# Optimization experiments

Measured on AMD Instinct MI355X. Metric: run time of the kernel, lower is better.

## Reference

```python
import jax, jax.numpy as jnp
import numpy as np
import math

TOKEN_DIM = 1024
NUM_HEADS = 16
HEAD_DIM = TOKEN_DIM // NUM_HEADS
T, B, N = 32, 32, 64


def setup_inputs() -> dict:
    key = jax.random.key(0)
    ks = jax.random.split(key, 9)
    query_vec = jax.random.normal(ks[0], (T, B, TOKEN_DIM), dtype=jnp.float32)
    tokens = jax.random.normal(ks[1], (T, B, N, TOKEN_DIM), dtype=jnp.float32)
    gate_logits = jax.random.normal(ks[2], (T, B, N), dtype=jnp.float32)
    scale = 1.0 / math.sqrt(TOKEN_DIM)
    Wq = jax.random.normal(ks[3], (TOKEN_DIM, TOKEN_DIM), dtype=jnp.float32) * scale
    Wk = jax.random.normal(ks[4], (TOKEN_DIM, TOKEN_DIM), dtype=jnp.float32) * scale
    Wv = jax.random.normal(ks[5], (TOKEN_DIM, TOKEN_DIM), dtype=jnp.float32) * scale
    bq = jnp.zeros((TOKEN_DIM,), dtype=jnp.float32)
    bk = jnp.zeros((TOKEN_DIM,), dtype=jnp.float32)
    bv = jnp.zeros((TOKEN_DIM,), dtype=jnp.float32)
    return {"query_vec": query_vec, "tokens": tokens, "gate_logits": gate_logits,
            "Wq": Wq, "bq": bq, "Wk": Wk, "bk": bk, "Wv": Wv, "bv": bv}


def reference(query_vec, tokens, gate_logits, Wq, bq, Wk, bk, Wv, bv):
    # QKV projections
    q = query_vec @ Wq + bq                      # [T,B,D]
    k = tokens @ Wk + bk                         # [T,B,N,D]
    v = tokens @ Wv + bv                         # [T,B,N,D]
    q = q.reshape(T, B, NUM_HEADS, HEAD_DIM)
    k = k.reshape(T, B, N, NUM_HEADS, HEAD_DIM)
    v = v.reshape(T, B, N, NUM_HEADS, HEAD_DIM)
    logits = jnp.einsum('tbhd,tbnhd->tbhn', q, k) / math.sqrt(HEAD_DIM)
    logits = logits + gate_logits[:, :, None, :]
    attn = jax.nn.softmax(logits, axis=-1)       # [T,B,H,N]
    attended = jnp.einsum('tbhn,tbnhd->tbhd', attn, v)
    attended = attended.reshape(T, B, TOKEN_DIM)
    mean_attn = attn.mean(axis=2)                # [T,B,N]
    return (attended, mean_attn, logits)
```

## Files before the change

### kernel.cpp

```cpp
#include <hip/hip_runtime.h>
#include <hip/hip_bf16.h>
#include <hip/hip_cooperative_groups.h>

namespace cg = cooperative_groups;

typedef __attribute__((ext_vector_type(4))) float f32x4;
typedef __attribute__((ext_vector_type(8))) short bf16x8;
typedef unsigned int u32;
typedef unsigned short u16;

#define DEV static __device__ __forceinline__


DEV u16 f2bf(float x){
  union { float f; u32 u; } v; v.f = x;
  u32 r = v.u + 0x7FFFu + ((v.u >> 16) & 1u);
  return (u16)(r >> 16);
}
DEV float bf2f(u16 s){
  union { u32 u; float f; } v; v.u = ((u32)s) << 16;
  return v.f;
}

#define MFMA16(a,b,c) __builtin_amdgcn_mfma_f32_16x16x32_bf16((a),(b),(c),0,0,0)

DEV int tok_off(int n, int dbyte){ return n*2048 + (dbyte ^ ((n & 7) << 4)); }

#define SWZ(n) ((((n)&3)<<5) | ((((n)>>2)&1)<<4))

DEV void bar_lgkm(){
  __builtin_amdgcn_sched_barrier(0);
  asm volatile("s_waitcnt lgkmcnt(0)" ::: "memory");
  __builtin_amdgcn_s_barrier();
  __builtin_amdgcn_sched_barrier(0);
}

DEV bf16x8 cvt8(f32x4 lo, f32x4 hi){
  union { u32 u[4]; bf16x8 v; } r;
  asm("v_cvt_pk_bf16_f32 %0, %1, %2" : "=v"(r.u[0]) : "v"(lo.x), "v"(lo.y));
  asm("v_cvt_pk_bf16_f32 %0, %1, %2" : "=v"(r.u[1]) : "v"(lo.z), "v"(lo.w));
  asm("v_cvt_pk_bf16_f32 %0, %1, %2" : "=v"(r.u[2]) : "v"(hi.x), "v"(hi.y));
  asm("v_cvt_pk_bf16_f32 %0, %1, %2" : "=v"(r.u[3]) : "v"(hi.z), "v"(hi.w));
  return r.v;
}

DEV void stage8(const float* __restrict__ tokens, int tbn, int tk0,
                char* smem, int bb, int w, int l){
  char* ldsb = smem + (size_t)bb*32768 + (size_t)w*8192;
  const char* gb = (const char*)tokens + (size_t)tbn*262144 + (size_t)tk0*4096;
  #pragma unroll
  for (int j = 0; j < 8; ++j){
    const int nloc  = w*2 + (j >> 2);
    const int inner = (((j & 3)*1024) + l*16) ^ SWZ(nloc);
    __builtin_amdgcn_global_load_lds(
        (const __attribute__((address_space(1))) u32*)(gb + (size_t)nloc*4096 + inner),
        (__attribute__((address_space(3))) u32*)(ldsb + j*1024),
        16, 0, 0);
  }
}

#define MEGA_DYN_LDS 65536

__global__ __launch_bounds__(256, 2) void k_mega(
    const float* __restrict__ qv, const float* __restrict__ tokens,
    const float* __restrict__ gate,
    const float* __restrict__ Wq, const float* __restrict__ bq,
    const float* __restrict__ Wk, const float* __restrict__ bk,
    const float* __restrict__ Wv, const float* __restrict__ bv,
    u16* __restrict__ qvB, u16* __restrict__ WqT, u16* __restrict__ WkB,
    u16* __restrict__ WvT, float* __restrict__ qf, u16* __restrict__ qb,
    u16* __restrict__ U, u16* __restrict__ ctxb,
    float* __restrict__ out_att, float* __restrict__ out_mean,
    float* __restrict__ out_logits){
  extern __shared__ __align__(16) char smem[];
  __shared__ __align__(16) char sstat[10496];
  cg::grid_group grid = cg::this_grid();
  const int tid = threadIdx.x;
  const int bx  = blockIdx.x;
  const int l = tid & 63, w = tid >> 6, g = l >> 4, li = l & 15;

  {
    const f32x4* s4 = (const f32x4*)qv;
    uint2* d2 = (uint2*)qvB;
    int g0 = bx*256 + tid;
    #pragma unroll
    for (int i = 0; i < 2; ++i){
      int idx = g0 + i*131072;
      f32x4 v = s4[idx];
      uint2 pk;
      pk.x = (u32)f2bf(v.x) | ((u32)f2bf(v.y) << 16);
      pk.y = (u32)f2bf(v.z) | ((u32)f2bf(v.w) << 16);
      d2[idx] = pk;
    }
  }
  {
    u16 (*tile)[65] = (u16 (*)[65])sstat;
    for (int tl = bx; tl < 768; tl += 512){
      __syncthreads();
      const int which = tl >> 8, t8 = tl & 255;
      const float* src = which==0 ? Wq : (which==1 ? Wk : Wv);
      const int bi = (t8 >> 4) << 6, bj = (t8 & 15) << 6;
      #pragma unroll
      for (int k2 = 0; k2 < 16; ++k2){
        int e = tid + (k2 << 8); int r = e >> 6, c = e & 63;
        tile[r][c] = f2bf(src[(size_t)(bi + r)*1024 + bj + c]);
      }
      __syncthreads();
      if (which == 1){
        #pragma unroll
        for (int k2 = 0; k2 < 16; ++k2){
          int e = tid + (k2 << 8); int r = e >> 6, c = e & 63;
          WkB[(size_t)(bi + r)*1024 + bj + c] = tile[r][c];
        }
      } else {
        u16* dst = which==0 ? WqT : WvT;
        #pragma unroll
        for (int k2 = 0; k2 < 16; ++k2){
          int e = tid + (k2 << 8); int r = e >> 6, c = e & 63;
          dst[(size_t)(bj + r)*1024 + bi + c] = tile[c][r];
        }
      }
    }
  }
  __threadfence(); grid.sync(); __threadfence();

  {
    const int wm = w & 1, wn = w >> 1;
    const int m_base = (bx >> 5)*64 + wm*32;
    const int n_base = (bx & 31)*32 + wn*16;
    f32x4 acc[2]; acc[0] = (f32x4)0.0f; acc[1] = (f32x4)0.0f;
    #pragma unroll 4
    for (int kb = 0; kb < 32; ++kb){
      const int k0 = kb*32 + g*8;
      bf16x8 b = *(const bf16x8*)(WqT + (size_t)(n_base + li)*1024 + k0);
      #pragma unroll
      for (int rt = 0; rt < 2; ++rt){
        bf16x8 a = *(const bf16x8*)(qvB + (size_t)(m_base + rt*16 + li)*1024 + k0);
        acc[rt] = MFMA16(a, b, acc[rt]);
      }
    }
    #pragma unroll
    for (int rt = 0; rt < 2; ++rt)
      #pragma unroll
      for (int r = 0; r < 4; ++r){
        int m = m_base + rt*16 + g*4 + r;
        int n = n_base + li;
        float val = acc[rt][r] + bq[n];
        qf[(size_t)m*1024 + n] = val;
        qb[(size_t)m*1024 + n] = f2bf(val);
      }
  }
  __threadfence(); grid.sync(); __threadfence();

  {
    u16 (*stile)[64] = (u16 (*)[64])sstat;
    const int wm = w & 1, wn = w >> 1;
    for (int i = 0; i < 8; ++i){
      const int tl = bx*8 + i;
      const int tb0 = (tl >> 8)*64, d0 = ((tl >> 4) & 15)*64, h = tl & 15;
      f32x4 acc[2][2];
      #pragma unroll
      for (int a0=0;a0<2;++a0)
        #pragma unroll
        for (int b0=0;b0<2;++b0) acc[a0][b0] = (f32x4)0.0f;
      #pragma unroll
      for (int kb = 0; kb < 2; ++kb){
        const int k0 = h*64 + kb*32 + g*8;
        bf16x8 a[2], b[2];
        #pragma unroll
        for (int rt=0;rt<2;++rt)
          a[rt] = *(const bf16x8*)(qb + (size_t)(tb0 + wm*32 + rt*16 + li)*1024 + k0);
        #pragma unroll
        for (int ct=0;ct<2;++ct)
          b[ct] = *(const bf16x8*)(WkB + (size_t)(d0 + wn*32 + ct*16 + li)*1024 + k0);
        #pragma unroll
        for (int rt=0;rt<2;++rt)
          #pragma unroll
          for (int ct=0;ct<2;++ct)
            acc[rt][ct] = MFMA16(a[rt], b[ct], acc[rt][ct]);
      }
      __syncthreads();
      #pragma unroll
      for (int rt=0;rt<2;++rt)
        #pragma unroll
        for (int ct=0;ct<2;++ct)
          #pragma unroll
          for (int r=0;r<4;++r)
            stile[wm*32 + rt*16 + g*4 + r][wn*32 + ct*16 + li] = f2bf(acc[rt][ct][r]);
      __syncthreads();
      const int rr = tid >> 2, cg4 = tid & 3;
      f32x4* dst = (f32x4*)(U + ((size_t)(tb0 + rr)*16 + h)*1024 + d0 + cg4*16);
      const f32x4* s4 = (const f32x4*)(&stile[rr][cg4*16]);
      dst[0] = s4[0]; dst[1] = s4[1];
    }
  }
  __threadfence(); grid.sync(); __threadfence();

  {
    float* part_s   = (float*)(sstat);
    float* logits_s = (float*)(sstat + 4096);
    float* p_s      = (float*)(sstat + 8192);
    float* csum     = (float*)(sstat + 10240);
    float* r_s      = (float*)(sstat + 10304);
    float* mzs      = (float*)(sstat + 10368);
    const int sh = tid >> 4, sj = tid & 15;

    __syncthreads();
    stage8(tokens, bx, 0, smem, 0, w, l);

    float m_run = -1e30f, z_run = 0.0f;
    f32x4 cacc[4][4];
    bf16x8 a[8];

    for (int r = 0; r < 16; ++r){
      const int c = r & 7, n0 = c*8;
      const int tb = bx + (r >> 3)*512;
      char* bufc = smem + (size_t)(r & 1)*32768;

      __syncthreads();
      if (r + 1 < 16)
        stage8(tokens, bx + ((r+1) >> 3)*512, ((r+1) & 7)*8, smem, (r+1) & 1, w, l);

      if (c == 0){
        m_run = -1e30f; z_run = 0.0f;
        #pragma unroll
        for (int i=0;i<4;++i)
          #pragma unroll
          for (int j=0;j<4;++j) cacc[i][j] = (f32x4)0.0f;
        const bf16x8* Ub = (const bf16x8*)(U + (size_t)tb*16384);
        #pragma unroll
        for (int i = 0; i < 8; ++i)
          a[i] = Ub[li*128 + (w*8 + i)*4 + g];
        const float* qp = qf + (size_t)tb*1024 + sh*64 + sj*4;
        const float* bp = bk + sh*64 + sj*4;
        float part = qp[0]*bp[0] + qp[1]*bp[1] + qp[2]*bp[2] + qp[3]*bp[3];
        part += __shfl_xor(part, 1); part += __shfl_xor(part, 2);
        part += __shfl_xor(part, 4); part += __shfl_xor(part, 8);
        if (sj == 0) csum[sh] = part;
      }

      {
        const int row = li & 7;
        const int sw  = SWZ(row);
        f32x4 acc = (f32x4)0.0f;
        #pragma unroll
        for (int i = 0; i < 8; ++i){
          const int p0b = (w*8 + i)*128 + g*32;
          f32x4 lo = *(const f32x4*)(bufc + row*4096 + ((p0b     ) ^ sw));
          f32x4 hi = *(const f32x4*)(bufc + row*4096 + ((p0b + 16) ^ sw));
          acc = MFMA16(a[i], cvt8(lo, hi), acc);
        }
        *(f32x4*)(part_s + (size_t)(w*64 + l)*4) = acc;
      }
      bar_lgkm();

      if (sj < 8){
        const int idx = ((sh >> 2)*16 + sj)*4 + (sh & 3);
        float lv = part_s[idx] + part_s[256 + idx] + part_s[512 + idx] + part_s[768 + idx];
        lv = (lv + csum[sh])*0.125f + gate[(size_t)tb*64 + n0 + sj];
        logits_s[sh*64 + n0 + sj] = lv;
        out_logits[(size_t)tb*1024 + sh*64 + n0 + sj] = lv;
        float cm = lv;
        cm = fmaxf(cm, __shfl_xor(cm, 1));
        cm = fmaxf(cm, __shfl_xor(cm, 2));
        cm = fmaxf(cm, __shfl_xor(cm, 4));
        float m_new = fmaxf(m_run, cm);
        float rsc = __expf(m_run - m_new);
        float p0 = __expf(lv - m_new);
        float zs = p0;
        zs += __shfl_xor(zs, 1); zs += __shfl_xor(zs, 2); zs += __shfl_xor(zs, 4);
        z_run = z_run * rsc + zs;
        m_run = m_new;
        p_s[sj*16 + sh] = p0;
        if (sj == 0){
          r_s[sh] = rsc;
          if (c == 7){ mzs[sh*2] = m_new; mzs[sh*2 + 1] = 1.0f / z_run; }
        }
      }
      bar_lgkm();

      {
        float rr4[4];
        #pragma unroll
        for (int hh = 0; hh < 4; ++hh) rr4[hh] = r_s[w*4 + hh];
        #pragma unroll
        for (int dq = 0; dq < 4; ++dq)
          #pragma unroll
          for (int hh = 0; hh < 4; ++hh) cacc[dq][hh] *= rr4[hh];
        #pragma unroll
        for (int nl = 0; nl < 8; ++nl){
          const f32x4 p = *(const f32x4*)(p_s + nl*16 + w*4);
          const int swn = SWZ(nl);
          #pragma unroll
          for (int dq = 0; dq < 4; ++dq){
            const f32x4 t = *(const f32x4*)(bufc + (size_t)nl*4096 + ((dq*1024 + l*16) ^ swn));
            #pragma unroll
            for (int hh = 0; hh < 4; ++hh)
              cacc[dq][hh] += t * p[hh];
          }
        }
      }

      if (c == 7){
        if (tid < 64){
          float s = 0.0f;
          #pragma unroll
          for (int h = 0; h < 16; ++h)
            s += __expf(logits_s[h*64 + tid] - mzs[h*2]) * mzs[h*2 + 1];
          out_mean[(size_t)tb*64 + tid] = s * 0.0625f;
        }
        #pragma unroll
        for (int hh = 0; hh < 4; ++hh){
          const int h = w*4 + hh;
          const float zinv = mzs[h*2 + 1];
          #pragma unroll
          for (int dq = 0; dq < 4; ++dq){
            f32x4 v = cacc[dq][hh];
            uint2 pk;
            pk.x = (u32)f2bf(v.x * zinv) | ((u32)f2bf(v.y * zinv) << 16);
            pk.y = (u32)f2bf(v.z * zinv) | ((u32)f2bf(v.w * zinv) << 16);
            *(uint2*)(ctxb + ((size_t)tb*16 + h)*1024 + dq*256 + l*4) = pk;
          }
        }
      }
    }
  }
  __threadfence(); grid.sync(); __threadfence();

  {
    const int wm = w & 1, wn = w >> 1;
    const int m_base = (bx >> 4)*32, h = bx & 15;
    f32x4 acc[2]; acc[0] = (f32x4)0.0f; acc[1] = (f32x4)0.0f;
    #pragma unroll 4
    for (int kb = 0; kb < 32; ++kb){
      const int k0 = kb*32 + g*8;
      bf16x8 a = *(const bf16x8*)(ctxb + ((size_t)(m_base + wm*16 + li)*16 + h)*1024 + k0);
      #pragma unroll
      for (int ct = 0; ct < 2; ++ct){
        bf16x8 b = *(const bf16x8*)(WvT + (size_t)(h*64 + wn*32 + ct*16 + li)*1024 + k0);
        acc[ct] = MFMA16(a, b, acc[ct]);
      }
    }
    #pragma unroll
    for (int ct = 0; ct < 2; ++ct)
      #pragma unroll
      for (int r = 0; r < 4; ++r){
        int m = m_base + wm*16 + g*4 + r;
        int dout = h*64 + wn*32 + ct*16 + li;
        out_att[(size_t)m*1024 + dout] = acc[ct][r] + bv[dout];
      }
  }
}

__global__ __launch_bounds__(256) void k_convert(
    const float* __restrict__ Wq, const float* __restrict__ Wk, const float* __restrict__ Wv,
    u16* __restrict__ WqT, u16* __restrict__ WkB, u16* __restrict__ WvT){
  __shared__ u16 tile[64][65];
  const int which = blockIdx.y;
  const float* src = which==0 ? Wq : (which==1 ? Wk : Wv);
  const int bi = (blockIdx.x >> 4) << 6;
  const int bj = (blockIdx.x & 15) << 6;
  const int t  = threadIdx.x;
  #pragma unroll
  for (int k2 = 0; k2 < 16; ++k2){
    int e = t + (k2 << 8);
    int r = e >> 6, c = e & 63;
    tile[r][c] = f2bf(src[(size_t)(bi + r)*1024 + bj + c]);
  }
  __syncthreads();
  if (which == 1){
    #pragma unroll
    for (int k2 = 0; k2 < 16; ++k2){
      int e = t + (k2 << 8); int r = e >> 6, c = e & 63;
      WkB[(size_t)(bi + r)*1024 + bj + c] = tile[r][c];
    }
  } else {
    u16* dst = which==0 ? WqT : WvT;
    #pragma unroll
    for (int k2 = 0; k2 < 16; ++k2){
      int e = t + (k2 << 8); int r = e >> 6, c = e & 63;
      dst[(size_t)(bj + r)*1024 + bi + c] = tile[c][r];
    }
  }
}

__global__ __launch_bounds__(256) void k_qproj(
    const float* __restrict__ qv, const u16* __restrict__ WqT, const float* __restrict__ bq,
    float* __restrict__ qf, u16* __restrict__ qb){
  const int l = threadIdx.x & 63, w = threadIdx.x >> 6;
  const int wm = w & 1, wn = w >> 1;
  const int g = l >> 4, li = l & 15;
  const int m_base = blockIdx.x*64 + wm*32;
  const int n_base = blockIdx.y*64 + wn*32;
  f32x4 acc[2][2];
  #pragma unroll
  for (int i=0;i<2;++i)
    #pragma unroll
    for (int j=0;j<2;++j) acc[i][j] = (f32x4)0.0f;

  #pragma unroll 4
  for (int kb = 0; kb < 32; ++kb){
    const int k0 = kb*32 + g*8;
    bf16x8 a[2], b[2];
    #pragma unroll
    for (int rt = 0; rt < 2; ++rt){
      const float* p = qv + (size_t)(m_base + rt*16 + li)*1024 + k0;
      f32x4 lo = *(const f32x4*)p;
      f32x4 hi = *(const f32x4*)(p+4);
      union { u16 s[8]; bf16x8 v; } u;
      u.s[0]=f2bf(lo.x); u.s[1]=f2bf(lo.y); u.s[2]=f2bf(lo.z); u.s[3]=f2bf(lo.w);
      u.s[4]=f2bf(hi.x); u.s[5]=f2bf(hi.y); u.s[6]=f2bf(hi.z); u.s[7]=f2bf(hi.w);
      a[rt] = u.v;
    }
    #pragma unroll
    for (int ct = 0; ct < 2; ++ct)
      b[ct] = *(const bf16x8*)(WqT + (size_t)(n_base + ct*16 + li)*1024 + k0);
    #pragma unroll
    for (int rt = 0; rt < 2; ++rt)
      #pragma unroll
      for (int ct = 0; ct < 2; ++ct)
        acc[rt][ct] = MFMA16(a[rt], b[ct], acc[rt][ct]);
  }
  #pragma unroll
  for (int rt=0;rt<2;++rt)
    #pragma unroll
    for (int ct=0;ct<2;++ct)
      #pragma unroll
      for (int r=0;r<4;++r){
        int m = m_base + rt*16 + g*4 + r;
        int n = n_base + ct*16 + li;
        float val = acc[rt][ct][r] + bq[n];
        qf[(size_t)m*1024 + n] = val;
        qb[(size_t)m*1024 + n] = f2bf(val);
      }
}

__global__ __launch_bounds__(256) void k_umat(
    const u16* __restrict__ qb, const u16* __restrict__ WkB, u16* __restrict__ U){
  __shared__ __align__(16) u16 stile[64][64];
  const int l = threadIdx.x & 63, w = threadIdx.x >> 6;
  const int wm = w & 1, wn = w >> 1, g = l >> 4, li = l & 15;
  const int tb0 = blockIdx.x*64, d0 = blockIdx.y*64, h = blockIdx.z;
  f32x4 acc[2][2];
  #pragma unroll
  for (int i=0;i<2;++i)
    #pragma unroll
    for (int j=0;j<2;++j) acc[i][j] = (f32x4)0.0f;

  #pragma unroll
  for (int kb = 0; kb < 2; ++kb){
    const int k0 = h*64 + kb*32 + g*8;
    bf16x8 a[2], b[2];
    #pragma unroll
    for (int rt=0;rt<2;++rt)
      a[rt] = *(const bf16x8*)(qb + (size_t)(tb0 + wm*32 + rt*16 + li)*1024 + k0);
    #pragma unroll
    for (int ct=0;ct<2;++ct)
      b[ct] = *(const bf16x8*)(WkB + (size_t)(d0 + wn*32 + ct*16 + li)*1024 + k0);
    #pragma unroll
    for (int rt=0;rt<2;++rt)
      #pragma unroll
      for (int ct=0;ct<2;++ct)
        acc[rt][ct] = MFMA16(a[rt], b[ct], acc[rt][ct]);
  }
  #pragma unroll
  for (int rt=0;rt<2;++rt)
    #pragma unroll
    for (int ct=0;ct<2;++ct)
      #pragma unroll
      for (int r=0;r<4;++r)
        stile[wm*32 + rt*16 + g*4 + r][wn*32 + ct*16 + li] = f2bf(acc[rt][ct][r]);
  __syncthreads();
  const int r = threadIdx.x >> 2, cg4 = threadIdx.x & 3;
  f32x4* dst = (f32x4*)(U + ((size_t)(tb0 + r)*16 + h)*1024 + d0 + cg4*16);
  const f32x4* s4 = (const f32x4*)(&stile[r][cg4*16]);
  dst[0] = s4[0]; dst[1] = s4[1];
}

#define K3_LDS 76032
__global__ __launch_bounds__(256, 2) void k_attn(
    const float* __restrict__ tokens, const float* __restrict__ gate,
    const u16* __restrict__ U, const float* __restrict__ qf, const float* __restrict__ bk,
    float* __restrict__ out_logits, float* __restrict__ out_mean, u16* __restrict__ ctx){
  extern __shared__ __align__(16) char smem[];
  float* part_s   = (float*)(smem + 65536);
  float* logits_s = (float*)(smem + 69632);
  float* p_s      = (float*)(smem + 73728);
  float* csum     = (float*)(smem + 75776);
  float* r_s      = (float*)(smem + 75840);
  float* mzs      = (float*)(smem + 75904);
  const int tb = blockIdx.x;
  const int tid = threadIdx.x;
  const int l = tid & 63, w = tid >> 6, g = l >> 4, li = l & 15;
  const int nt = w & 1, kh = w >> 1;
  const int sh = tid >> 4, sj = tid & 15;

  bf16x8 a[16];
  const bf16x8* Ub = (const bf16x8*)(U + (size_t)tb*16384);
  #pragma unroll
  for (int i = 0; i < 16; ++i)
    a[i] = Ub[li*128 + (kh*16 + i)*4 + g];

  {
    const float* qp = qf + (size_t)tb*1024 + sh*64 + sj*4;
    const float* bp = bk + sh*64 + sj*4;
    float part = qp[0]*bp[0] + qp[1]*bp[1] + qp[2]*bp[2] + qp[3]*bp[3];
    part += __shfl_xor(part, 1); part += __shfl_xor(part, 2);
    part += __shfl_xor(part, 4); part += __shfl_xor(part, 8);
    if (sj == 0) csum[sh] = part;
  }

  float m_run = -1e30f, z_run = 0.0f;
  f32x4 cacc[4][4];
  #pragma unroll
  for (int i=0;i<4;++i)
    #pragma unroll
    for (int j=0;j<4;++j) cacc[i][j] = (f32x4)0.0f;

  const f32x4* src4 = (const f32x4*)(tokens + (size_t)tb*65536);

  for (int c = 0; c < 2; ++c){
    const int n0 = c*32;
    __syncthreads();
    #pragma unroll 8
    for (int it = 0; it < 32; ++it){
      f32x4 v = src4[(size_t)(n0 + it)*256 + tid];
      uint2 pk;
      pk.x = (u32)f2bf(v.x) | ((u32)f2bf(v.y) << 16);
      pk.y = (u32)f2bf(v.z) | ((u32)f2bf(v.w) << 16);
      *(uint2*)(smem + tok_off(it, tid*8)) = pk;
    }
    __syncthreads();
    {
      f32x4 acc = (f32x4)0.0f;
      #pragma unroll
      for (int i = 0; i < 16; ++i){
        int kb = kh*16 + i;
        bf16x8 b = *(const bf16x8*)(smem + tok_off(nt*16 + li, (kb*32 + g*8)*2));
        acc = MFMA16(a[i], b, acc);
      }
      *(f32x4*)(part_s + (size_t)(w*64 + l)*4) = acc;
      __syncthreads();
      if (kh == 0){
        acc += *(const f32x4*)(part_s + (size_t)((w+2)*64 + l)*4);
        float gv = gate[(size_t)tb*64 + n0 + nt*16 + li];
        #pragma unroll
        for (int r = 0; r < 4; ++r){
          int h = g*4 + r;
          logits_s[h*64 + n0 + nt*16 + li] = (acc[r] + csum[h])*0.125f + gv;
        }
      }
      __syncthreads();
    }
    {
      float lv0 = logits_s[sh*64 + n0 + sj];
      float lv1 = logits_s[sh*64 + n0 + 16 + sj];
      out_logits[(size_t)tb*1024 + sh*64 + n0 + sj]      = lv0;
      out_logits[(size_t)tb*1024 + sh*64 + n0 + 16 + sj] = lv1;
      float cm = fmaxf(lv0, lv1);
      cm = fmaxf(cm, __shfl_xor(cm, 1)); cm = fmaxf(cm, __shfl_xor(cm, 2));
      cm = fmaxf(cm, __shfl_xor(cm, 4)); cm = fmaxf(cm, __shfl_xor(cm, 8));
      float m_new = fmaxf(m_run, cm);
      float rsc = __expf(m_run - m_new);
      float p0 = __expf(lv0 - m_new), p1 = __expf(lv1 - m_new);
      float zs = p0 + p1;
      zs += __shfl_xor(zs, 1); zs += __shfl_xor(zs, 2);
      zs += __shfl_xor(zs, 4); zs += __shfl_xor(zs, 8);
      z_run = z_run * rsc + zs;
      m_run = m_new;
      p_s[sj*16 + sh]        = p0;
      p_s[(sj + 16)*16 + sh] = p1;
      if (sj == 0){
        r_s[sh] = rsc;
        if (c == 1){ mzs[sh*2] = m_new; mzs[sh*2 + 1] = 1.0f / z_run; }
      }
    }
    __syncthreads();
    {
      float rr[4];
      #pragma unroll
      for (int hh = 0; hh < 4; ++hh) rr[hh] = r_s[w*4 + hh];
      #pragma unroll
      for (int dq = 0; dq < 4; ++dq)
        #pragma unroll
        for (int hh = 0; hh < 4; ++hh) cacc[dq][hh] *= rr[hh];
      for (int nl = 0; nl < 32; ++nl){
        f32x4 p = *(const f32x4*)(p_s + nl*16 + w*4);
        #pragma unroll
        for (int dq = 0; dq < 4; ++dq){
          uint2 t2 = *(const uint2*)(smem + tok_off(nl, (dq*256 + l*4)*2));
          float f0 = bf2f((u16)(t2.x & 0xFFFFu));
          float f1 = bf2f((u16)(t2.x >> 16));
          float f2 = bf2f((u16)(t2.y & 0xFFFFu));
          float f3 = bf2f((u16)(t2.y >> 16));
          #pragma unroll
          for (int hh = 0; hh < 4; ++hh){
            float av = p[hh];
            cacc[dq][hh].x += av*f0; cacc[dq][hh].y += av*f1;
            cacc[dq][hh].z += av*f2; cacc[dq][hh].w += av*f3;
          }
        }
      }
    }
  }

  if (tid < 64){
    float s = 0.0f;
    #pragma unroll
    for (int h = 0; h < 16; ++h)
      s += __expf(logits_s[h*64 + tid] - mzs[h*2]) * mzs[h*2 + 1];
    out_mean[(size_t)tb*64 + tid] = s * 0.0625f;
  }

  #pragma unroll
  for (int hh = 0; hh < 4; ++hh){
    const int h = w*4 + hh;
    const float zinv = mzs[h*2 + 1];
    #pragma unroll
    for (int dq = 0; dq < 4; ++dq){
      f32x4 v = cacc[dq][hh];
      uint2 pk;
      pk.x = (u32)f2bf(v.x * zinv) | ((u32)f2bf(v.y * zinv) << 16);
      pk.y = (u32)f2bf(v.z * zinv) | ((u32)f2bf(v.w * zinv) << 16);
      *(uint2*)(ctx + ((size_t)tb*16 + h)*1024 + dq*256 + l*4) = pk;
    }
  }
}

__global__ __launch_bounds__(256) void k_attended(
    const u16* __restrict__ ctx, const u16* __restrict__ WvT, const float* __restrict__ bv,
    float* __restrict__ out_att){
  const int l = threadIdx.x & 63, w = threadIdx.x >> 6;
  const int wm = w & 1, wn = w >> 1, g = l >> 4, li = l & 15;
  const int tb0 = blockIdx.x*64, h = blockIdx.y;
  f32x4 acc[2][2];
  #pragma unroll
  for (int i=0;i<2;++i)
    #pragma unroll
    for (int j=0;j<2;++j) acc[i][j] = (f32x4)0.0f;

  #pragma unroll 4
  for (int kb = 0; kb < 32; ++kb){
    const int k0 = kb*32 + g*8;
    bf16x8 a[2], b[2];
    #pragma unroll
    for (int rt=0;rt<2;++rt)
      a[rt] = *(const bf16x8*)(ctx + ((size_t)(tb0 + wm*32 + rt*16 + li)*16 + h)*1024 + k0);
    #pragma unroll
    for (int ct=0;ct<2;++ct)
      b[ct] = *(const bf16x8*)(WvT + (size_t)(h*64 + wn*32 + ct*16 + li)*1024 + k0);
    #pragma unroll
    for (int rt=0;rt<2;++rt)
      #pragma unroll
      for (int ct=0;ct<2;++ct)
        acc[rt][ct] = MFMA16(a[rt], b[ct], acc[rt][ct]);
  }
  #pragma unroll
  for (int rt=0;rt<2;++rt)
    #pragma unroll
    for (int ct=0;ct<2;++ct)
      #pragma unroll
      for (int r=0;r<4;++r){
        int m = tb0 + wm*32 + rt*16 + g*4 + r;
        int dout = h*64 + wn*32 + ct*16 + li;
        out_att[(size_t)m*1024 + dout] = acc[rt][ct][r] + bv[dout];
      }
}

extern "C" void kernel_launch(void* const* d_in, const int* in_sizes, int n_in,
                              void* d_out, int out_size, void* d_ws, size_t ws_size,
                              hipStream_t stream){
  const float* qv     = (const float*)d_in[0];
  const float* tokens = (const float*)d_in[1];
  const float* gate   = (const float*)d_in[2];
  const float* Wq     = (const float*)d_in[3];
  const float* bq     = (const float*)d_in[4];
  const float* Wk     = (const float*)d_in[5];
  const float* bk     = (const float*)d_in[6];
  const float* Wv     = (const float*)d_in[7];
  const float* bv     = (const float*)d_in[8];

  char* ws = (char*)d_ws;
  u16*   qvB = (u16*)(ws);
  u16*   WqT = (u16*)(ws + (2u<<20));
  u16*   WkB = (u16*)(ws + (4u<<20));
  u16*   WvT = (u16*)(ws + (6u<<20));
  float* qf  = (float*)(ws + (8u<<20));
  u16*   qb  = (u16*)(ws + (12u<<20));
  u16*   U   = (u16*)(ws + (14u<<20));
  u16*   ctxb= (u16*)(ws + (46u<<20));

  float* out_att    = (float*)d_out;
  float* out_mean   = out_att + 1048576;
  float* out_logits = out_att + 1114112;

  int dev = 0; (void)hipGetDevice(&dev);
  int coop = 0; (void)hipDeviceGetAttribute(&coop, hipDeviceAttributeCooperativeLaunch, dev);
  int ncu = 0;  (void)hipDeviceGetAttribute(&ncu, hipDeviceAttributeMultiprocessorCount, dev);
  int perCU = 0;
  hipError_t oe = hipOccupancyMaxActiveBlocksPerMultiprocessor(
                      &perCU, (const void*)k_mega, 256, (size_t)MEGA_DYN_LDS);
  bool use_coop = (coop != 0) && (oe == hipSuccess) && ((long)perCU * (long)ncu >= 512);

  if (use_coop){
    void* args[] = { (void*)&qv, (void*)&tokens, (void*)&gate,
                     (void*)&Wq, (void*)&bq, (void*)&Wk, (void*)&bk,
                     (void*)&Wv, (void*)&bv,
                     (void*)&qvB, (void*)&WqT, (void*)&WkB, (void*)&WvT,
                     (void*)&qf, (void*)&qb, (void*)&U, (void*)&ctxb,
                     (void*)&out_att, (void*)&out_mean, (void*)&out_logits };
    hipError_t le = hipLaunchCooperativeKernel((const void*)k_mega, dim3(512), dim3(256),
                                               args, MEGA_DYN_LDS, stream);
    if (le == hipSuccess) return;
    use_coop = false;
  }

  (void)hipFuncSetAttribute((const void*)k_attn,
                            hipFuncAttributeMaxDynamicSharedMemorySize, K3_LDS);
  k_convert <<<dim3(256, 3),    256, 0,      stream>>>(Wq, Wk, Wv, WqT, WkB, WvT);
  k_qproj   <<<dim3(16, 16),    256, 0,      stream>>>(qv, WqT, bq, qf, qb);
  k_umat    <<<dim3(16, 16, 16),256, 0,      stream>>>(qb, WkB, U);
  k_attn    <<<dim3(1024),      256, K3_LDS, stream>>>(tokens, gate, U, qf, bk,
                                                       out_logits, out_mean, ctxb);
  k_attended<<<dim3(16, 16),    256, 0,      stream>>>(ctxb, WvT, bv, out_att);
}
```

Baseline: 177.3 us.

## Replace cooperative megakernel with multi-kernel path using async fp32 token staging

Removes the cooperative-launch megakernel and its grid-wide syncs, so the separate kernel sequence (convert, qproj, umat, attn, attended) always runs. The k_attn kernel now streams fp32 tokens into a double-buffered LDS with direct global-to-LDS loads in 8-token chunks and converts to bf16 inside the MFMA path, instead of converting synchronously in 32-token chunks. Each block now handles one tb rather than two in a persistent loop, with more blocks in flight. The trade-off is extra kernel launch boundaries in place of grid syncs.

```diff
diff --git a/kernel.cpp b/kernel.cpp
--- a/kernel.cpp
+++ b/kernel.cpp
@@ -1,8 +1,5 @@
 #include <hip/hip_runtime.h>
 #include <hip/hip_bf16.h>
-#include <hip/hip_cooperative_groups.h>
-
-namespace cg = cooperative_groups;
 
 typedef __attribute__((ext_vector_type(4))) float f32x4;
 typedef __attribute__((ext_vector_type(8))) short bf16x8;
@@ -24,13 +21,17 @@
 
 #define MFMA16(a,b,c) __builtin_amdgcn_mfma_f32_16x16x32_bf16((a),(b),(c),0,0,0)
 
-DEV int tok_off(int n, int dbyte){ return n*2048 + (dbyte ^ ((n & 7) << 4)); }
-
 #define SWZ(n) ((((n)&3)<<5) | ((((n)>>2)&1)<<4))
 
 DEV void bar_lgkm(){
   __builtin_amdgcn_sched_barrier(0);
   asm volatile("s_waitcnt lgkmcnt(0)" ::: "memory");
+  __builtin_amdgcn_s_barrier();
+  __builtin_amdgcn_sched_barrier(0);
+}
+DEV void bar_full(){
+  __builtin_amdgcn_sched_barrier(0);
+  asm volatile("s_waitcnt vmcnt(0) lgkmcnt(0)" ::: "memory");
   __builtin_amdgcn_s_barrier();
   __builtin_amdgcn_sched_barrier(0);
 }
@@ -56,299 +57,6 @@
         (const __attribute__((address_space(1))) u32*)(gb + (size_t)nloc*4096 + inner),
         (__attribute__((address_space(3))) u32*)(ldsb + j*1024),
         16, 0, 0);
-  }
-}
-
-#define MEGA_DYN_LDS 65536
-
-__global__ __launch_bounds__(256, 2) void k_mega(
-    const float* __restrict__ qv, const float* __restrict__ tokens,
-    const float* __restrict__ gate,
-    const float* __restrict__ Wq, const float* __restrict__ bq,
-    const float* __restrict__ Wk, const float* __restrict__ bk,
-    const float* __restrict__ Wv, const float* __restrict__ bv,
-    u16* __restrict__ qvB, u16* __restrict__ WqT, u16* __restrict__ WkB,
-    u16* __restrict__ WvT, float* __restrict__ qf, u16* __restrict__ qb,
-    u16* __restrict__ U, u16* __restrict__ ctxb,
-    float* __restrict__ out_att, float* __restrict__ out_mean,
-    float* __restrict__ out_logits){
-  extern __shared__ __align__(16) char smem[];
-  __shared__ __align__(16) char sstat[10496];
-  cg::grid_group grid = cg::this_grid();
-  const int tid = threadIdx.x;
-  const int bx  = blockIdx.x;
-  const int l = tid & 63, w = tid >> 6, g = l >> 4, li = l & 15;
-
-  {
-    const f32x4* s4 = (const f32x4*)qv;
-    uint2* d2 = (uint2*)qvB;
-    int g0 = bx*256 + tid;
-    #pragma unroll
-    for (int i = 0; i < 2; ++i){
-      int idx = g0 + i*131072;
-      f32x4 v = s4[idx];
-      uint2 pk;
-      pk.x = (u32)f2bf(v.x) | ((u32)f2bf(v.y) << 16);
-      pk.y = (u32)f2bf(v.z) | ((u32)f2bf(v.w) << 16);
-      d2[idx] = pk;
-    }
-  }
-  {
-    u16 (*tile)[65] = (u16 (*)[65])sstat;
-    for (int tl = bx; tl < 768; tl += 512){
-      __syncthreads();
-      const int which = tl >> 8, t8 = tl & 255;
-      const float* src = which==0 ? Wq : (which==1 ? Wk : Wv);
-      const int bi = (t8 >> 4) << 6, bj = (t8 & 15) << 6;
-      #pragma unroll
-      for (int k2 = 0; k2 < 16; ++k2){
-        int e = tid + (k2 << 8); int r = e >> 6, c = e & 63;
-        tile[r][c] = f2bf(src[(size_t)(bi + r)*1024 + bj + c]);
-      }
-      __syncthreads();
-      if (which == 1){
-        #pragma unroll
-        for (int k2 = 0; k2 < 16; ++k2){
-          int e = tid + (k2 << 8); int r = e >> 6, c = e & 63;
-          WkB[(size_t)(bi + r)*1024 + bj + c] = tile[r][c];
-        }
-      } else {
-        u16* dst = which==0 ? WqT : WvT;
-        #pragma unroll
-        for (int k2 = 0; k2 < 16; ++k2){
-          int e = tid + (k2 << 8); int r = e >> 6, c = e & 63;
-          dst[(size_t)(bj + r)*1024 + bi + c] = tile[c][r];
-        }
-      }
-    }
-  }
-  __threadfence(); grid.sync(); __threadfence();
-
-  {
-    const int wm = w & 1, wn = w >> 1;
-    const int m_base = (bx >> 5)*64 + wm*32;
-    const int n_base = (bx & 31)*32 + wn*16;
-    f32x4 acc[2]; acc[0] = (f32x4)0.0f; acc[1] = (f32x4)0.0f;
-    #pragma unroll 4
-    for (int kb = 0; kb < 32; ++kb){
-      const int k0 = kb*32 + g*8;
-      bf16x8 b = *(const bf16x8*)(WqT + (size_t)(n_base + li)*1024 + k0);
-      #pragma unroll
-      for (int rt = 0; rt < 2; ++rt){
-        bf16x8 a = *(const bf16x8*)(qvB + (size_t)(m_base + rt*16 + li)*1024 + k0);
-        acc[rt] = MFMA16(a, b, acc[rt]);
-      }
-    }
-    #pragma unroll
-    for (int rt = 0; rt < 2; ++rt)
-      #pragma unroll
-      for (int r = 0; r < 4; ++r){
-        int m = m_base + rt*16 + g*4 + r;
-        int n = n_base + li;
-        float val = acc[rt][r] + bq[n];
-        qf[(size_t)m*1024 + n] = val;
-        qb[(size_t)m*1024 + n] = f2bf(val);
-      }
-  }
-  __threadfence(); grid.sync(); __threadfence();
-
-  {
-    u16 (*stile)[64] = (u16 (*)[64])sstat;
-    const int wm = w & 1, wn = w >> 1;
-    for (int i = 0; i < 8; ++i){
-      const int tl = bx*8 + i;
-      const int tb0 = (tl >> 8)*64, d0 = ((tl >> 4) & 15)*64, h = tl & 15;
-      f32x4 acc[2][2];
-      #pragma unroll
-      for (int a0=0;a0<2;++a0)
-        #pragma unroll
-        for (int b0=0;b0<2;++b0) acc[a0][b0] = (f32x4)0.0f;
-      #pragma unroll
-      for (int kb = 0; kb < 2; ++kb){
-        const int k0 = h*64 + kb*32 + g*8;
-        bf16x8 a[2], b[2];
-        #pragma unroll
-        for (int rt=0;rt<2;++rt)
-          a[rt] = *(const bf16x8*)(qb + (size_t)(tb0 + wm*32 + rt*16 + li)*1024 + k0);
-        #pragma unroll
-        for (int ct=0;ct<2;++ct)
-          b[ct] = *(const bf16x8*)(WkB + (size_t)(d0 + wn*32 + ct*16 + li)*1024 + k0);
-        #pragma unroll
-        for (int rt=0;rt<2;++rt)
-          #pragma unroll
-          for (int ct=0;ct<2;++ct)
-            acc[rt][ct] = MFMA16(a[rt], b[ct], acc[rt][ct]);
-      }
-      __syncthreads();
-      #pragma unroll
-      for (int rt=0;rt<2;++rt)
-        #pragma unroll
-        for (int ct=0;ct<2;++ct)
-          #pragma unroll
-          for (int r=0;r<4;++r)
-            stile[wm*32 + rt*16 + g*4 + r][wn*32 + ct*16 + li] = f2bf(acc[rt][ct][r]);
-      __syncthreads();
-      const int rr = tid >> 2, cg4 = tid & 3;
-      f32x4* dst = (f32x4*)(U + ((size_t)(tb0 + rr)*16 + h)*1024 + d0 + cg4*16);
-      const f32x4* s4 = (const f32x4*)(&stile[rr][cg4*16]);
-      dst[0] = s4[0]; dst[1] = s4[1];
-    }
-  }
-  __threadfence(); grid.sync(); __threadfence();
-
-  {
-    float* part_s   = (float*)(sstat);
-    float* logits_s = (float*)(sstat + 4096);
-    float* p_s      = (float*)(sstat + 8192);
-    float* csum     = (float*)(sstat + 10240);
-    float* r_s      = (float*)(sstat + 10304);
-    float* mzs      = (float*)(sstat + 10368);
-    const int sh = tid >> 4, sj = tid & 15;
-
-    __syncthreads();
-    stage8(tokens, bx, 0, smem, 0, w, l);
-
-    float m_run = -1e30f, z_run = 0.0f;
-    f32x4 cacc[4][4];
-    bf16x8 a[8];
-
-    for (int r = 0; r < 16; ++r){
-      const int c = r & 7, n0 = c*8;
-      const int tb = bx + (r >> 3)*512;
-      char* bufc = smem + (size_t)(r & 1)*32768;
-
-      __syncthreads();
-      if (r + 1 < 16)
-        stage8(tokens, bx + ((r+1) >> 3)*512, ((r+1) & 7)*8, smem, (r+1) & 1, w, l);
-
-      if (c == 0){
-        m_run = -1e30f; z_run = 0.0f;
-        #pragma unroll
-        for (int i=0;i<4;++i)
-          #pragma unroll
-          for (int j=0;j<4;++j) cacc[i][j] = (f32x4)0.0f;
-        const bf16x8* Ub = (const bf16x8*)(U + (size_t)tb*16384);
-        #pragma unroll
-        for (int i = 0; i < 8; ++i)
-          a[i] = Ub[li*128 + (w*8 + i)*4 + g];
-        const float* qp = qf + (size_t)tb*1024 + sh*64 + sj*4;
-        const float* bp = bk + sh*64 + sj*4;
-        float part = qp[0]*bp[0] + qp[1]*bp[1] + qp[2]*bp[2] + qp[3]*bp[3];
-        part += __shfl_xor(part, 1); part += __shfl_xor(part, 2);
-        part += __shfl_xor(part, 4); part += __shfl_xor(part, 8);
-        if (sj == 0) csum[sh] = part;
-      }
-
-      {
-        const int row = li & 7;
-        const int sw  = SWZ(row);
-        f32x4 acc = (f32x4)0.0f;
-        #pragma unroll
-        for (int i = 0; i < 8; ++i){
-          const int p0b = (w*8 + i)*128 + g*32;
-          f32x4 lo = *(const f32x4*)(bufc + row*4096 + ((p0b     ) ^ sw));
-          f32x4 hi = *(const f32x4*)(bufc + row*4096 + ((p0b + 16) ^ sw));
-          acc = MFMA16(a[i], cvt8(lo, hi), acc);
-        }
-        *(f32x4*)(part_s + (size_t)(w*64 + l)*4) = acc;
-      }
-      bar_lgkm();
-
-      if (sj < 8){
-        const int idx = ((sh >> 2)*16 + sj)*4 + (sh & 3);
-        float lv = part_s[idx] + part_s[256 + idx] + part_s[512 + idx] + part_s[768 + idx];
-        lv = (lv + csum[sh])*0.125f + gate[(size_t)tb*64 + n0 + sj];
-        logits_s[sh*64 + n0 + sj] = lv;
-        out_logits[(size_t)tb*1024 + sh*64 + n0 + sj] = lv;
-        float cm = lv;
-        cm = fmaxf(cm, __shfl_xor(cm, 1));
-        cm = fmaxf(cm, __shfl_xor(cm, 2));
-        cm = fmaxf(cm, __shfl_xor(cm, 4));
-        float m_new = fmaxf(m_run, cm);
-        float rsc = __expf(m_run - m_new);
-        float p0 = __expf(lv - m_new);
-        float zs = p0;
-        zs += __shfl_xor(zs, 1); zs += __shfl_xor(zs, 2); zs += __shfl_xor(zs, 4);
-        z_run = z_run * rsc + zs;
-        m_run = m_new;
-        p_s[sj*16 + sh] = p0;
-        if (sj == 0){
-          r_s[sh] = rsc;
-          if (c == 7){ mzs[sh*2] = m_new; mzs[sh*2 + 1] = 1.0f / z_run; }
-        }
-      }
-      bar_lgkm();
-
-      {
-        float rr4[4];
-        #pragma unroll
-        for (int hh = 0; hh < 4; ++hh) rr4[hh] = r_s[w*4 + hh];
-        #pragma unroll
-        for (int dq = 0; dq < 4; ++dq)
-          #pragma unroll
-          for (int hh = 0; hh < 4; ++hh) cacc[dq][hh] *= rr4[hh];
-        #pragma unroll
-        for (int nl = 0; nl < 8; ++nl){
-          const f32x4 p = *(const f32x4*)(p_s + nl*16 + w*4);
-          const int swn = SWZ(nl);
-          #pragma unroll
-          for (int dq = 0; dq < 4; ++dq){
-            const f32x4 t = *(const f32x4*)(bufc + (size_t)nl*4096 + ((dq*1024 + l*16) ^ swn));
-            #pragma unroll
-            for (int hh = 0; hh < 4; ++hh)
-              cacc[dq][hh] += t * p[hh];
-          }
-        }
-      }
-
-      if (c == 7){
-        if (tid < 64){
-          float s = 0.0f;
-          #pragma unroll
-          for (int h = 0; h < 16; ++h)
-            s += __expf(logits_s[h*64 + tid] - mzs[h*2]) * mzs[h*2 + 1];
-          out_mean[(size_t)tb*64 + tid] = s * 0.0625f;
-        }
-        #pragma unroll
-        for (int hh = 0; hh < 4; ++hh){
-          const int h = w*4 + hh;
-          const float zinv = mzs[h*2 + 1];
-          #pragma unroll
-          for (int dq = 0; dq < 4; ++dq){
-            f32x4 v = cacc[dq][hh];
-            uint2 pk;
-            pk.x = (u32)f2bf(v.x * zinv) | ((u32)f2bf(v.y * zinv) << 16);
-            pk.y = (u32)f2bf(v.z * zinv) | ((u32)f2bf(v.w * zinv) << 16);
-            *(uint2*)(ctxb + ((size_t)tb*16 + h)*1024 + dq*256 + l*4) = pk;
-          }
-        }
-      }
-    }
-  }
-  __threadfence(); grid.sync(); __threadfence();
-
-  {
-    const int wm = w & 1, wn = w >> 1;
-    const int m_base = (bx >> 4)*32, h = bx & 15;
-    f32x4 acc[2]; acc[0] = (f32x4)0.0f; acc[1] = (f32x4)0.0f;
-    #pragma unroll 4
-    for (int kb = 0; kb < 32; ++kb){
-      const int k0 = kb*32 + g*8;
-      bf16x8 a = *(const bf16x8*)(ctxb + ((size_t)(m_base + wm*16 + li)*16 + h)*1024 + k0);
-      #pragma unroll
-      for (int ct = 0; ct < 2; ++ct){
-        bf16x8 b = *(const bf16x8*)(WvT + (size_t)(h*64 + wn*32 + ct*16 + li)*1024 + k0);
-        acc[ct] = MFMA16(a, b, acc[ct]);
-      }
-    }
-    #pragma unroll
-    for (int ct = 0; ct < 2; ++ct)
-      #pragma unroll
-      for (int r = 0; r < 4; ++r){
-        int m = m_base + wm*16 + g*4 + r;
-        int dout = h*64 + wn*32 + ct*16 + li;
-        out_att[(size_t)m*1024 + dout] = acc[ct][r] + bv[dout];
-      }
   }
 }
 
@@ -477,29 +185,29 @@
   dst[0] = s4[0]; dst[1] = s4[1];
 }
 
-#define K3_LDS 76032
+#define K3_LDS 65536
 __global__ __launch_bounds__(256, 2) void k_attn(
     const float* __restrict__ tokens, const float* __restrict__ gate,
     const u16* __restrict__ U, const float* __restrict__ qf, const float* __restrict__ bk,
     float* __restrict__ out_logits, float* __restrict__ out_mean, u16* __restrict__ ctx){
   extern __shared__ __align__(16) char smem[];
-  float* part_s   = (float*)(smem + 65536);
-  float* logits_s = (float*)(smem + 69632);
-  float* p_s      = (float*)(smem + 73728);
-  float* csum     = (float*)(smem + 75776);
-  float* r_s      = (float*)(smem + 75840);
-  float* mzs      = (float*)(smem + 75904);
+  __shared__ __align__(16) char sstat[8960];
+  float* part_s   = (float*)(sstat);
+  float* logits_s = (float*)(sstat + 4096);
+  float* p_s      = (float*)(sstat + 8192);
+  float* csum     = (float*)(sstat + 8704);
+  float* r_s      = (float*)(sstat + 8768);
+  float* mzs      = (float*)(sstat + 8832);
   const int tb = blockIdx.x;
   const int tid = threadIdx.x;
   const int l = tid & 63, w = tid >> 6, g = l >> 4, li = l & 15;
-  const int nt = w & 1, kh = w >> 1;
   const int sh = tid >> 4, sj = tid & 15;
 
-  bf16x8 a[16];
+  bf16x8 a[8];
   const bf16x8* Ub = (const bf16x8*)(U + (size_t)tb*16384);
   #pragma unroll
-  for (int i = 0; i < 16; ++i)
-    a[i] = Ub[li*128 + (kh*16 + i)*4 + g];
+  for (int i = 0; i < 8; ++i)
+    a[i] = Ub[li*128 + (w*8 + i)*4 + g];
 
   {
     const float* qp = qf + (size_t)tb*1024 + sh*64 + sj*4;
@@ -517,88 +225,74 @@
     #pragma unroll
     for (int j=0;j<4;++j) cacc[i][j] = (f32x4)0.0f;
 
-  const f32x4* src4 = (const f32x4*)(tokens + (size_t)tb*65536);
-
-  for (int c = 0; c < 2; ++c){
-    const int n0 = c*32;
-    __syncthreads();
-    #pragma unroll 8
-    for (int it = 0; it < 32; ++it){
-      f32x4 v = src4[(size_t)(n0 + it)*256 + tid];
-      uint2 pk;
-      pk.x = (u32)f2bf(v.x) | ((u32)f2bf(v.y) << 16);
-      pk.y = (u32)f2bf(v.z) | ((u32)f2bf(v.w) << 16);
-      *(uint2*)(smem + tok_off(it, tid*8)) = pk;
-    }
-    __syncthreads();
+  stage8(tokens, tb, 0, smem, 0, w, l);
+
+  for (int r = 0; r < 8; ++r){
+    const int n0 = r*8;
+    char* bufc = smem + (size_t)(r & 1)*32768;
+
+    bar_full();
+    if (r + 1 < 8)
+      stage8(tokens, tb, (r+1)*8, smem, (r+1) & 1, w, l);
+
     {
+      const int row = li & 7;
+      const int sw  = SWZ(row);
       f32x4 acc = (f32x4)0.0f;
       #pragma unroll
-      for (int i = 0; i < 16; ++i){
-        int kb = kh*16 + i;
-        bf16x8 b = *(const bf16x8*)(smem + tok_off(nt*16 + li, (kb*32 + g*8)*2));
-        acc = MFMA16(a[i], b, acc);
+      for (int i = 0; i < 8; ++i){
+        const int p0b = (w*8 + i)*128 + g*32;
+        f32x4 lo = *(const f32x4*)(bufc + row*4096 + ((p0b     ) ^ sw));
+        f32x4 hi = *(const f32x4*)(bufc + row*4096 + ((p0b + 16) ^ sw));
+        acc = MFMA16(a[i], cvt8(lo, hi), acc);
       }
       *(f32x4*)(part_s + (size_t)(w*64 + l)*4) = acc;
-      __syncthreads();
-      if (kh == 0){
-        acc += *(const f32x4*)(part_s + (size_t)((w+2)*64 + l)*4);
-        float gv = gate[(size_t)tb*64 + n0 + nt*16 + li];
-        #pragma unroll
-        for (int r = 0; r < 4; ++r){
-          int h = g*4 + r;
-          logits_s[h*64 + n0 + nt*16 + li] = (acc[r] + csum[h])*0.125f + gv;
-        }
-      }
-      __syncthreads();
-    }
-    {
-      float lv0 = logits_s[sh*64 + n0 + sj];
-      float lv1 = logits_s[sh*64 + n0 + 16 + sj];
-      out_logits[(size_t)tb*1024 + sh*64 + n0 + sj]      = lv0;
-      out_logits[(size_t)tb*1024 + sh*64 + n0 + 16 + sj] = lv1;
-      float cm = fmaxf(lv0, lv1);
-      cm = fmaxf(cm, __shfl_xor(cm, 1)); cm = fmaxf(cm, __shfl_xor(cm, 2));
-      cm = fmaxf(cm, __shfl_xor(cm, 4)); cm = fmaxf(cm, __shfl_xor(cm, 8));
+    }
+    bar_lgkm();
+
+    if (sj < 8){
+      const int idx = ((sh >> 2)*16 + sj)*4 + (sh & 3);
+      float lv = part_s[idx] + part_s[256 + idx] + part_s[512 + idx] + part_s[768 + idx];
+      lv = (lv + csum[sh])*0.125f + gate[(size_t)tb*64 + n0 + sj];
+      logits_s[sh*64 + n0 + sj] = lv;
+      out_logits[(size_t)tb*1024 + sh*64 + n0 + sj] = lv;
+      float cm = lv;
+      cm = fmaxf(cm, __shfl_xor(cm, 1));
+      cm = fmaxf(cm, __shfl_xor(cm, 2));
+      cm = fmaxf(cm, __shfl_xor(cm, 4));
       float m_new = fmaxf(m_run, cm);
       float rsc = __expf(m_run - m_new);
-      float p0 = __expf(lv0 - m_new), p1 = __expf(lv1 - m_new);
-      float zs = p0 + p1;
-      zs += __shfl_xor(zs, 1); zs += __shfl_xor(zs, 2);
-      zs += __shfl_xor(zs, 4); zs += __shfl_xor(zs, 8);
+      float p0 = __expf(lv - m_new);
+      float zs = p0;
+      zs += __shfl_xor(zs, 1); zs += __shfl_xor(zs, 2); zs += __shfl_xor(zs, 4);
       z_run = z_run * rsc + zs;
       m_run = m_new;
-      p_s[sj*16 + sh]        = p0;
-      p_s[(sj + 16)*16 + sh] = p1;
+      p_s[sj*16 + sh] = p0;
       if (sj == 0){
         r_s[sh] = rsc;
-        if (c == 1){ mzs[sh*2] = m_new; mzs[sh*2 + 1] = 1.0f / z_run; }
-      }
-    }
-    __syncthreads();
+        if (r == 7){ mzs[sh*2] = m_new; mzs[sh*2 + 1] = 1.0f / z_run; }
+      }
+    }
+    bar_lgkm();
+
     {
-      float rr[4];
-      #pragma unroll
-      for (int hh = 0; hh < 4; ++hh) rr[hh] = r_s[w*4 + hh];
+      float rr4[4];
+      #pragma unroll
+      for (int hh = 0; hh < 4; ++hh) rr4[hh] = r_s[w*4 + hh];
       #pragma unroll
       for (int dq = 0; dq < 4; ++dq)
         #pragma unroll
-        for (int hh = 0; hh < 4; ++hh) cacc[dq][hh] *= rr[hh];
-      for (int nl = 0; nl < 32; ++nl){
-        f32x4 p = *(const f32x4*)(p_s + nl*16 + w*4);
+        for (int hh = 0; hh < 4; ++hh) cacc[dq][hh] *= rr4[hh];
+      #pragma unroll
+      for (int nl = 0; nl < 8; ++nl){
+        const f32x4 p = *(const f32x4*)(p_s + nl*16 + w*4);
+        const int swn = SWZ(nl);
         #pragma unroll
         for (int dq = 0; dq < 4; ++dq){
-          uint2 t2 = *(const uint2*)(smem + tok_off(nl, (dq*256 + l*4)*2));
-          float f0 = bf2f((u16)(t2.x & 0xFFFFu));
-          float f1 = bf2f((u16)(t2.x >> 16));
-          float f2 = bf2f((u16)(t2.y & 0xFFFFu));
-          float f3 = bf2f((u16)(t2.y >> 16));
+          const f32x4 t = *(const f32x4*)(bufc + (size_t)nl*4096 + ((dq*1024 + l*16) ^ swn));
           #pragma unroll
-          for (int hh = 0; hh < 4; ++hh){
-            float av = p[hh];
-            cacc[dq][hh].x += av*f0; cacc[dq][hh].y += av*f1;
-            cacc[dq][hh].z += av*f2; cacc[dq][hh].w += av*f3;
-          }
+          for (int hh = 0; hh < 4; ++hh)
+            cacc[dq][hh] += t * p[hh];
         }
       }
     }
@@ -611,7 +305,6 @@
       s += __expf(logits_s[h*64 + tid] - mzs[h*2]) * mzs[h*2 + 1];
     out_mean[(size_t)tb*64 + tid] = s * 0.0625f;
   }
-
   #pragma unroll
   for (int hh = 0; hh < 4; ++hh){
     const int h = w*4 + hh;
@@ -681,39 +374,17 @@
   const float* bv     = (const float*)d_in[8];
 
   char* ws = (char*)d_ws;
-  u16*   qvB = (u16*)(ws);
-  u16*   WqT = (u16*)(ws + (2u<<20));
-  u16*   WkB = (u16*)(ws + (4u<<20));
-  u16*   WvT = (u16*)(ws + (6u<<20));
-  float* qf  = (float*)(ws + (8u<<20));
-  u16*   qb  = (u16*)(ws + (12u<<20));
-  u16*   U   = (u16*)(ws + (14u<<20));
-  u16*   ctxb= (u16*)(ws + (46u<<20));
+  u16*   WqT = (u16*)(ws);
+  u16*   WkB = (u16*)(ws + (2u<<20));
+  u16*   WvT = (u16*)(ws + (4u<<20));
+  float* qf  = (float*)(ws + (6u<<20));
+  u16*   qb  = (u16*)(ws + (10u<<20));
+  u16*   U   = (u16*)(ws + (12u<<20));
+  u16*   ctxb= (u16*)(ws + (44u<<20));
 
   float* out_att    = (float*)d_out;
   float* out_mean   = out_att + 1048576;
   float* out_logits = out_att + 1114112;
-
-  int dev = 0; (void)hipGetDevice(&dev);
-  int coop = 0; (void)hipDeviceGetAttribute(&coop, hipDeviceAttributeCooperativeLaunch, dev);
-  int ncu = 0;  (void)hipDeviceGetAttribute(&ncu, hipDeviceAttributeMultiprocessorCount, dev);
-  int perCU = 0;
-  hipError_t oe = hipOccupancyMaxActiveBlocksPerMultiprocessor(
-                      &perCU, (const void*)k_mega, 256, (size_t)MEGA_DYN_LDS);
-  bool use_coop = (coop != 0) && (oe == hipSuccess) && ((long)perCU * (long)ncu >= 512);
-
-  if (use_coop){
-    void* args[] = { (void*)&qv, (void*)&tokens, (void*)&gate,
-                     (void*)&Wq, (void*)&bq, (void*)&Wk, (void*)&bk,
-                     (void*)&Wv, (void*)&bv,
-                     (void*)&qvB, (void*)&WqT, (void*)&WkB, (void*)&WvT,
-                     (void*)&qf, (void*)&qb, (void*)&U, (void*)&ctxb,
-                     (void*)&out_att, (void*)&out_mean, (void*)&out_logits };
-    hipError_t le = hipLaunchCooperativeKernel((const void*)k_mega, dim3(512), dim3(256),
-                                               args, MEGA_DYN_LDS, stream);
-    if (le == hipSuccess) return;
-    use_coop = false;
-  }
 
   (void)hipFuncSetAttribute((const void*)k_attn,
                             hipFuncAttributeMaxDynamicSharedMemorySize, K3_LDS);
```

Result: faster. 160.2 us (-9.7%).
